# Kernel optimization log

Hardware: AMD Instinct MI355X
Metric: run time of the kernel (lower is better)

Reference implementation:

```python
import jax, jax.numpy as jnp
import numpy as np

N, NN = 16384, 10          # n_messages, max neighbors
IN, H = 135, 256           # input feature size, hidden size
HEADS, DPH = 4, 256 // 4   # attention heads, dim per head
DEPTH = 5
NEG_INF = -1e18


def setup_inputs() -> dict:
    key = jax.random.key(0)
    ks = jax.random.split(key, 17)
    s = lambda k, sh: (jax.random.normal(k, sh, jnp.float32) * 0.05)
    return {
        "fmess": jax.random.normal(ks[0], (N, IN), jnp.float32),
        "bgraph": jax.random.randint(ks[1], (N, NN), 0, N),
        "Wq": s(ks[2], (H, IN)), "bq": s(ks[3], (H,)),
        "Wk": s(ks[4], (H, H)), "bk": s(ks[5], (H,)),
        "Wv": s(ks[6], (H, H)), "bv": s(ks[7], (H,)),
        "alpha": s(ks[8], (1, 1, HEADS, 2 * DPH)),
        "abias": s(ks[9], (1, 1, HEADS)),
        "Wz": s(ks[10], (H, IN + H)), "bz": s(ks[11], (H,)),
        "Wr": s(ks[12], (H, IN)),
        "Ur": s(ks[13], (H, H)), "bur": s(ks[14], (H,)),
        "Wh": s(ks[15], (H, IN + H)), "bh": s(ks[16], (H,)),
    }


def reference(fmess, bgraph, Wq, bq, Wk, bk, Wv, bv, alpha, abias,
              Wz, bz, Wr, Ur, bur, Wh, bh):
    n = fmess.shape[0]
    # q depends only on fmess -> compute once (identical math to per-step recompute)
    q = (fmess @ Wq.T + bq).reshape(n, 1, HEADS, DPH)
    node_mask = jnp.ones((n, 1), jnp.float32).at[0, 0].set(0.0)

    def step(h, _):
        h_nei = h[bgraph]                                   # [n, nn, H] gather
        k = (h_nei @ Wk.T + bk).reshape(n, NN, HEADS, DPH)
        v = (h_nei @ Wv.T + bv).reshape(n, NN, HEADS, DPH)
        qb = jnp.broadcast_to(q, (n, NN, HEADS, DPH))
        qk = jax.nn.leaky_relu(jnp.concatenate([qb, k], axis=-1))  # slope 0.01
        score = jnp.sum(qk * alpha, axis=-1) + abias        # [n, nn, heads]
        attn_mask = (jnp.sum(h_nei, axis=2) == 0)[:, :, None]
        score = jnp.where(attn_mask, NEG_INF, score)
        w = jax.nn.softmax(score, axis=1)                   # softmax over neighbors
        sum_h = jnp.einsum('nmh,nmhd->nhd', w, v).reshape(n, H)
        z = jax.nn.sigmoid(jnp.concatenate([fmess, sum_h], axis=1) @ Wz.T + bz)
        r = jax.nn.sigmoid(fmess @ Wr.T + sum_h @ Ur.T + bur)
        pre_h = jnp.tanh(jnp.concatenate([fmess, r * sum_h], axis=1) @ Wh.T + bh)
        new_h = ((1.0 - z) * sum_h + z * pre_h) * node_mask
        return new_h, None

    h0 = jnp.zeros((n, H), jnp.float32)
    h, _ = jax.lax.scan(step, h0, None, length=DEPTH)
    return h
```

## Files before the change

### kernel.cpp

```cpp
#include <hip/hip_runtime.h>
#include <hip/hip_bf16.h>
#include <math.h>

#define NMSG 16384
#define NNEI 10
#define INF_ 135
#define KPAD 160
#define HID 256
#define DPH 64
#define DEPTH 5

typedef __attribute__((ext_vector_type(8))) short short8b;
typedef __attribute__((ext_vector_type(4))) float f32x4;
typedef __hip_bfloat16 bf16;

__device__ __forceinline__ float sigmoidf_(float x){ return 1.f/(1.f+expf(-x)); }
__device__ __forceinline__ float b2f(unsigned short u){ return __uint_as_float(((unsigned)u)<<16); }
__device__ __forceinline__ float ldb(const bf16* p, size_t off){
    return b2f(*((const unsigned short*)p + off));
}

__device__ __forceinline__ void gload_lds16(const void* g, void* l){
    __builtin_amdgcn_global_load_lds(
        (const __attribute__((address_space(1))) unsigned int*)g,
        (__attribute__((address_space(3))) unsigned int*)l, 16, 0, 0);
}

template<int EPI>
__global__ __launch_bounds__(256) void mm_k(
    const bf16* __restrict__ A1, const bf16* __restrict__ A2,
    const bf16* __restrict__ B1, const bf16* __restrict__ B2, int K,
    const bf16* __restrict__ E0, const bf16* __restrict__ E1,
    const float* __restrict__ b0, const float* __restrict__ b1,
    const bf16* __restrict__ SH,
    float* __restrict__ Cf, bf16* __restrict__ Cb0, bf16* __restrict__ Cb1, bf16* __restrict__ Cb2,
    const float* __restrict__ AL, float* __restrict__ SKout, float* __restrict__ Snext)
{
    constexpr int BM = (EPI==0) ? 128 : 64;
    constexpr int MF = BM/64;
    constexpr int BK = 32;
    constexpr bool DB = (EPI>=2);
    constexpr bool DA = (EPI==3);
    __shared__ __align__(16) unsigned short As1[BM*BK];
    __shared__ __align__(16) unsigned short As2[DA ? BM*BK : 8];
    __shared__ __align__(16) unsigned short Bs1[64*BK];
    __shared__ __align__(16) unsigned short Bs2[DB ? 64*BK : 8];
    const int tid = threadIdx.x;
    const int w = tid >> 6, lane = tid & 63;
    const int bm0 = blockIdx.x * BM;
    const int bn0 = blockIdx.y * 64;
    const int rq = lane >> 2, slot = lane & 3;
    const int fr = lane & 15, fs = lane >> 4;
    const int wrow = w * (MF*16);

    f32x4 acc1[MF][4] = {};
    f32x4 acc2[MF][4] = {};

    for (int k0 = 0; k0 < K; k0 += BK){
        #pragma unroll
        for (int i = 0; i < MF; ++i){
            const int r0 = i*64 + w*16;
            const int r  = r0 + rq;
            const int sw = slot ^ ((r >> 1) & 3);
            gload_lds16(A1 + (size_t)(bm0 + r)*K + k0 + sw*8, As1 + r0*BK);
            if constexpr (DA)
                gload_lds16(A2 + (size_t)(bm0 + r)*K + k0 + sw*8, As2 + r0*BK);
        }
        {
            const int r0 = w*16;
            const int r  = r0 + rq;
            const int sw = slot ^ ((r >> 1) & 3);
            gload_lds16(B1 + (size_t)(bn0 + r)*K + k0 + sw*8, Bs1 + r0*BK);
            if constexpr (DB)
                gload_lds16(B2 + (size_t)(bn0 + r)*K + k0 + sw*8, Bs2 + r0*BK);
        }
        __syncthreads();
        short8b af1[MF], af2[MF], bv1[4], bv2[4];
        #pragma unroll
        for (int mi = 0; mi < MF; ++mi){
            const int row = wrow + mi*16 + fr;
            const int sw = fs ^ ((row >> 1) & 3);
            af1[mi] = *(const short8b*)((const char*)As1 + row*64 + sw*16);
            if constexpr (DA)
                af2[mi] = *(const short8b*)((const char*)As2 + row*64 + sw*16);
        }
        #pragma unroll
        for (int ni = 0; ni < 4; ++ni){
            const int row = ni*16 + fr;
            const int sw = fs ^ ((row >> 1) & 3);
            bv1[ni] = *(const short8b*)((const char*)Bs1 + row*64 + sw*16);
            if constexpr (DB)
                bv2[ni] = *(const short8b*)((const char*)Bs2 + row*64 + sw*16);
        }
        #pragma unroll
        for (int mi = 0; mi < MF; ++mi)
            #pragma unroll
            for (int ni = 0; ni < 4; ++ni){
                acc1[mi][ni] = __builtin_amdgcn_mfma_f32_16x16x32_bf16(af1[mi], bv1[ni], acc1[mi][ni], 0, 0, 0);
                if constexpr (DB)
                    acc2[mi][ni] = __builtin_amdgcn_mfma_f32_16x16x32_bf16(
                        DA ? af2[mi] : af1[mi], bv2[ni], acc2[mi][ni], 0, 0, 0);
            }
        __syncthreads();
    }

    if constexpr (EPI == 0 || EPI == 1){
        const bool score = (EPI == 1) || (blockIdx.y < 4);
        if (score){
            const int head = blockIdx.y;
            #pragma unroll
            for (int mi = 0; mi < MF; ++mi){
                #pragma unroll
                for (int t = 0; t < 4; ++t){
                    float p = 0.f;
                    #pragma unroll
                    for (int ni = 0; ni < 4; ++ni){
                        const int d = ni*16 + fr;
                        float x = acc1[mi][ni][t] + b0[head*64 + d];
                        float lr = x > 0.f ? x : 0.01f*x;
                        p = fmaf(lr, AL[head*128 + d], p);
                    }
                    p += __shfl_xor(p,1); p += __shfl_xor(p,2);
                    p += __shfl_xor(p,4); p += __shfl_xor(p,8);
                    if (fr == 0){
                        const int m = bm0 + wrow + mi*16 + fs*4 + t;
                        SKout[m*4 + head] = p;
                    }
                }
            }
        } else {
            const int sel = ((int)blockIdx.y - 4) >> 2;
            bf16* dst = (sel == 0) ? Cb0 : (sel == 1) ? Cb1 : Cb2;
            const int cbase = (((int)blockIdx.y - 4) & 3) * 64;
            #pragma unroll
            for (int mi = 0; mi < MF; ++mi)
                #pragma unroll
                for (int ni = 0; ni < 4; ++ni)
                    #pragma unroll
                    for (int t = 0; t < 4; ++t){
                        const int m = bm0 + wrow + mi*16 + fs*4 + t;
                        const int c = cbase + ni*16 + fr;
                        dst[(size_t)m*HID + c] = __float2bfloat16(acc1[mi][ni][t]);
                    }
        }
    } else if constexpr (EPI == 2){
        const int cbase = (int)blockIdx.y * 64;
        #pragma unroll
        for (int mi = 0; mi < MF; ++mi)
            #pragma unroll
            for (int ni = 0; ni < 4; ++ni)
                #pragma unroll
                for (int t = 0; t < 4; ++t){
                    const int m = bm0 + wrow + mi*16 + fs*4 + t;
                    const int c = cbase + ni*16 + fr;
                    const size_t off = (size_t)m*HID + c;
                    const float sumh = acc1[mi][ni][t] + b0[c];
                    const float r = sigmoidf_(acc2[mi][ni][t] + ldb(E1, off) + b1[c]);
                    Cb0[off] = __float2bfloat16(sumh);
                    Cb1[off] = __float2bfloat16(r * sumh);
                }
    } else {
        const int cbase = (int)blockIdx.y * 64;
        #pragma unroll
        for (int mi = 0; mi < MF; ++mi){
            #pragma unroll
            for (int t = 0; t < 4; ++t){
                const int m = bm0 + wrow + mi*16 + fs*4 + t;
                float psum = 0.f;
                #pragma unroll
                for (int ni = 0; ni < 4; ++ni){
                    const int c = cbase + ni*16 + fr;
                    const size_t off = (size_t)m*HID + c;
                    const float ph = tanhf(acc1[mi][ni][t] + ldb(E0, off) + b0[c]);
                    const float z  = sigmoidf_(acc2[mi][ni][t] + ldb(E1, off) + b1[c]);
                    const float sh = ldb(SH, off);
                    float hn = (1.f - z)*sh + z*ph;
                    if (m == 0) hn = 0.f;
                    if (Cf)  Cf[off]  = hn;
                    if (Cb0) Cb0[off] = __float2bfloat16(hn);
                    psum += hn;
                }
                if (Snext){
                    psum += __shfl_xor(psum,1); psum += __shfl_xor(psum,2);
                    psum += __shfl_xor(psum,4); psum += __shfl_xor(psum,8);
                    if (fr == 0) atomicAdd(&Snext[m], psum);
                }
            }
        }
    }
}

struct ConvSegs {
    const float* src[8];
    bf16* dst[8];
    int srcld[8], col0[8], ncols[8], dstld[8];
    int start[8];
};
__global__ __launch_bounds__(256) void convall_k(ConvSegs cs, int total){
    int i = blockIdx.x*256 + threadIdx.x;
    if (i >= total) return;
    int s = 0;
    #pragma unroll
    for (int j = 1; j < 8; ++j) if (i >= cs.start[j]) s = j;
    const int li = i - cs.start[s];
    const int ld = cs.dstld[s];
    const int r = li / ld, c = li - r*ld;
    float v = (c < cs.ncols[s]) ? cs.src[s][(size_t)r*cs.srcld[s] + cs.col0[s] + c] : 0.f;
    cs.dst[s][li] = __float2bfloat16(v);
}

__global__ __launch_bounds__(256) void wcomb_k(
    const float* __restrict__ Ur, const float* __restrict__ Wz,
    const float* __restrict__ Wv, const float* __restrict__ bv,
    const float* __restrict__ bur, const float* __restrict__ bz,
    bf16* __restrict__ Urv, bf16* __restrict__ Wzv,
    float* __restrict__ bur2, float* __restrict__ bz2)
{
    const int i = blockIdx.x, j = threadIdx.x;
    const bool zp = (i >= 256);
    const int r = zp ? i - 256 : i;
    const float* Arow = zp ? (Wz + (size_t)r*(INF_+HID) + INF_) : (Ur + (size_t)r*HID);
    float acc = 0.f;
    for (int q = 0; q < HID; ++q)
        acc = fmaf(Arow[q], Wv[(size_t)q*HID + j], acc);
    (zp ? Wzv : Urv)[(size_t)r*HID + j] = __float2bfloat16(acc);
    float part = Arow[j] * bv[j];
    part += __shfl_xor(part,1);  part += __shfl_xor(part,2);  part += __shfl_xor(part,4);
    part += __shfl_xor(part,8);  part += __shfl_xor(part,16); part += __shfl_xor(part,32);
    __shared__ float red[4];
    if ((j & 63) == 0) red[j >> 6] = part;
    __syncthreads();
    if (j == 0){
        float s = red[0] + red[1] + red[2] + red[3];
        if (zp) bz2[r] = bz[r] + s; else bur2[r] = bur[r] + s;
    }
}

__global__ __launch_bounds__(256) void attn_k(
    const int*   __restrict__ bgraph,
    const float* __restrict__ sq,
    const float* __restrict__ sk,
    const float* __restrict__ S,
    const float* __restrict__ abias,
    const bf16*  __restrict__ H,
    bf16* __restrict__ haggb)
{
    const int gid  = blockIdx.x*256 + threadIdx.x;
    const int n    = gid >> 6;
    const int lane = gid & 63;
    const int head = lane >> 4;
    const float ab  = abias[head];
    const float sqv = sq[n*4 + head];
    int g[NNEI];
    #pragma unroll
    for (int j = 0; j < NNEI; ++j) g[j] = bgraph[n*NNEI + j];
    float sc[NNEI];
    float mx = -1e30f;
    #pragma unroll
    for (int j = 0; j < NNEI; ++j){
        float s = sqv + sk[g[j]*4 + head] + ab;
        if (S[g[j]] == 0.f) s = -1e18f;
        sc[j] = s;
        mx = fmaxf(mx, s);
    }
    float den = 0.f;
    #pragma unroll
    for (int j = 0; j < NNEI; ++j){ sc[j] = expf(sc[j] - mx); den += sc[j]; }
    const float inv = 1.f/den;
    float a0=0.f, a1=0.f, a2=0.f, a3=0.f;
    #pragma unroll
    for (int j = 0; j < NNEI; ++j){
        const float w = sc[j]*inv;
        const ushort4 vv = *reinterpret_cast<const ushort4*>(
            (const unsigned short*)H + (size_t)g[j]*HID + lane*4);
        a0 = fmaf(w, b2f(vv.x), a0);
        a1 = fmaf(w, b2f(vv.y), a1);
        a2 = fmaf(w, b2f(vv.z), a2);
        a3 = fmaf(w, b2f(vv.w), a3);
    }
    ushort4 ob;
    { bf16 t0=__float2bfloat16(a0); ob.x=*(unsigned short*)&t0; }
    { bf16 t1=__float2bfloat16(a1); ob.y=*(unsigned short*)&t1; }
    { bf16 t2=__float2bfloat16(a2); ob.z=*(unsigned short*)&t2; }
    { bf16 t3=__float2bfloat16(a3); ob.w=*(unsigned short*)&t3; }
    *reinterpret_cast<ushort4*>((unsigned short*)haggb + (size_t)n*HID + lane*4) = ob;
}

extern "C" void kernel_launch(void* const* d_in, const int* in_sizes, int n_in,
                              void* d_out, int out_size, void* d_ws, size_t ws_size,
                              hipStream_t stream) {
    const float* fmess = (const float*)d_in[0];
    const int*   bgraph= (const int*  )d_in[1];
    const float* Wq    = (const float*)d_in[2];
    const float* bq    = (const float*)d_in[3];
    const float* Wk    = (const float*)d_in[4];
    const float* bk    = (const float*)d_in[5];
    const float* Wv    = (const float*)d_in[6];
    const float* bv    = (const float*)d_in[7];
    const float* alpha = (const float*)d_in[8];
    const float* abias = (const float*)d_in[9];
    const float* Wz    = (const float*)d_in[10];
    const float* bz    = (const float*)d_in[11];
    const float* Wr    = (const float*)d_in[12];
    const float* Ur    = (const float*)d_in[13];
    const float* bur   = (const float*)d_in[14];
    const float* Wh    = (const float*)d_in[15];
    const float* bh    = (const float*)d_in[16];
    float* out = (float*)d_out;

    const size_t NH = (size_t)NMSG*HID;
    char* p = (char*)d_ws;
    auto alloc = [&](size_t bytes)->char*{ char* r = p; p += (bytes + 255) & ~(size_t)255; return r; };
    bf16* fmessb = (bf16*)alloc((size_t)NMSG*KPAD*2);
    bf16* Wcat   = (bf16*)alloc((size_t)1024*KPAD*2);
    bf16* Wkb    = (bf16*)alloc((size_t)256*HID*2);
    bf16* Wvb    = (bf16*)alloc((size_t)256*HID*2);
    bf16* Wh2b   = (bf16*)alloc((size_t)256*HID*2);
    bf16* Urv    = (bf16*)alloc((size_t)256*HID*2);
    bf16* Wzv    = (bf16*)alloc((size_t)256*HID*2);
    float* bur2  = (float*)alloc(256*4);
    float* bz2   = (float*)alloc(256*4);
    bf16* FZb    = (bf16*)alloc(NH*2);
    bf16* FRb    = (bf16*)alloc(NH*2);
    bf16* FHb    = (bf16*)alloc(NH*2);
    bf16* sumhb  = (bf16*)alloc(NH*2);
    bf16* rsb    = (bf16*)alloc(NH*2);
    char* zreg   = alloc(NH*2 + NH*2 + 5*(size_t)NMSG*4);
    bf16*  hb    = (bf16*)zreg;
    bf16*  haggb = (bf16*)(zreg + NH*2);
    float* S_all = (float*)(zreg + NH*2 + NH*2);
    const size_t zbytes = NH*2 + NH*2 + 5*(size_t)NMSG*4;
    float* sq    = (float*)alloc((size_t)NMSG*4*4);
    float* sk    = (float*)alloc((size_t)NMSG*4*4);

    const dim3 gb(256);
    const int rgrid = NMSG*64/256;

    {
        ConvSegs cs;
        const size_t WQK = (size_t)256*KPAD;
        const float* srcs[8] = {fmess, Wq, Wz, Wr, Wh, Wk, Wv, Wh};
        bf16* dsts[8] = {fmessb, Wcat, Wcat+WQK, Wcat+2*WQK, Wcat+3*WQK, Wkb, Wvb, Wh2b};
        int srclds[8] = {INF_, INF_, INF_+HID, INF_, INF_+HID, HID, HID, INF_+HID};
        int col0s[8]  = {0,0,0,0,0, 0,0,INF_};
        int ncolss[8] = {INF_,INF_,INF_,INF_,INF_, HID,HID,HID};
        int dstlds[8] = {KPAD,KPAD,KPAD,KPAD,KPAD, HID,HID,HID};
        int sizes[8]  = {NMSG*KPAD, 256*KPAD,256*KPAD,256*KPAD,256*KPAD,
                         256*HID,256*HID,256*HID};
        int st = 0;
        for (int j = 0; j < 8; ++j){
            cs.src[j]=srcs[j]; cs.dst[j]=dsts[j]; cs.srcld[j]=srclds[j];
            cs.col0[j]=col0s[j]; cs.ncols[j]=ncolss[j]; cs.dstld[j]=dstlds[j];
            cs.start[j]=st; st += sizes[j];
        }
        convall_k<<<(st+255)/256, gb, 0, stream>>>(cs, st);
    }
    wcomb_k<<<512, gb, 0, stream>>>(Ur, Wz, Wv, bv, bur, bz, Urv, Wzv, bur2, bz2);
    hipMemsetAsync(zreg, 0, zbytes, stream);

    mm_k<0><<<dim3(NMSG/128, 16), gb, 0, stream>>>(fmessb, nullptr, Wcat, nullptr, KPAD,
        nullptr, nullptr, bq, nullptr, nullptr,
        nullptr, FZb, FRb, FHb, alpha, sq, nullptr);

    for (int step = 0; step < DEPTH; ++step){
        const bool last = (step == DEPTH-1);
        float* cf    = last ? out : nullptr;
        bf16*  cb    = last ? nullptr : hb;
        float* Snext = last ? nullptr : (S_all + (step+1)*(size_t)NMSG);
        if (step > 0){
            mm_k<1><<<dim3(NMSG/64, 4), gb, 0, stream>>>(hb, nullptr, Wkb, nullptr, HID,
                nullptr, nullptr, bk, nullptr, nullptr,
                nullptr, nullptr, nullptr, nullptr, alpha + DPH, sk, nullptr);
            attn_k<<<rgrid, gb, 0, stream>>>(bgraph, sq, sk, S_all + step*(size_t)NMSG,
                                             abias, hb, haggb);
        }
        mm_k<2><<<dim3(NMSG/64, 4), gb, 0, stream>>>(haggb, nullptr, Wvb, Urv, HID,
            nullptr, FRb, bv, bur2, nullptr,
            nullptr, sumhb, rsb, nullptr, nullptr, nullptr, nullptr);
        mm_k<3><<<dim3(NMSG/64, 4), gb, 0, stream>>>(rsb, haggb, Wh2b, Wzv, HID,
            FHb, FZb, bh, bz2, sumhb,
            cf, cb, nullptr, nullptr, nullptr, nullptr, Snext);
    }
}
```

Before: 393.6 us.

## Fuse per-step kernels into one persistent kernel with grid barriers

Replaces the per-depth-step launches (K-score GEMM, attention gather, two gated GEMMs) with a single persistent kernel that loops over the steps and separates phases with atomic-counter grid barriers. The aim is to remove launch overhead and inter-kernel gaps across the roughly 15 dependent launches. In exchange, a fixed grid (occupancy × 256, capped at 512) does grid-stride tiles, and several barriers per step add spin-wait cost. Correctness relies on all blocks being co-resident, since the launch is not cooperative.

```diff
diff --git a/kernel.cpp b/kernel.cpp
--- a/kernel.cpp
+++ b/kernel.cpp
@@ -26,158 +26,299 @@
         (__attribute__((address_space(3))) unsigned int*)l, 16, 0, 0);
 }
 
-template<int EPI>
-__global__ __launch_bounds__(256) void mm_k(
-    const bf16* __restrict__ A1, const bf16* __restrict__ A2,
-    const bf16* __restrict__ B1, const bf16* __restrict__ B2, int K,
-    const bf16* __restrict__ E0, const bf16* __restrict__ E1,
-    const float* __restrict__ b0, const float* __restrict__ b1,
-    const bf16* __restrict__ SH,
-    float* __restrict__ Cf, bf16* __restrict__ Cb0, bf16* __restrict__ Cb1, bf16* __restrict__ Cb2,
-    const float* __restrict__ AL, float* __restrict__ SKout, float* __restrict__ Snext)
+__device__ __forceinline__ void gbar(unsigned* cnt, unsigned target){
+    __threadfence();
+    __syncthreads();
+    if (threadIdx.x == 0){
+        __hip_atomic_fetch_add(cnt, 1u, __ATOMIC_RELEASE, __HIP_MEMORY_SCOPE_AGENT);
+        unsigned v;
+        do {
+            __builtin_amdgcn_s_sleep(2);
+            v = __hip_atomic_load(cnt, __ATOMIC_ACQUIRE, __HIP_MEMORY_SCOPE_AGENT);
+        } while (v < target);
+    }
+    __syncthreads();
+    __threadfence();
+}
+
+__global__ __launch_bounds__(256) void pre_k(
+    const bf16* __restrict__ A1, const bf16* __restrict__ B1, int K,
+    const float* __restrict__ b0,
+    bf16* __restrict__ Cb0, bf16* __restrict__ Cb1, bf16* __restrict__ Cb2,
+    const float* __restrict__ AL, float* __restrict__ SKout)
 {
-    constexpr int BM = (EPI==0) ? 128 : 64;
-    constexpr int MF = BM/64;
-    constexpr int BK = 32;
-    constexpr bool DB = (EPI>=2);
-    constexpr bool DA = (EPI==3);
+    constexpr int BM=128, BK=32;
     __shared__ __align__(16) unsigned short As1[BM*BK];
-    __shared__ __align__(16) unsigned short As2[DA ? BM*BK : 8];
     __shared__ __align__(16) unsigned short Bs1[64*BK];
-    __shared__ __align__(16) unsigned short Bs2[DB ? 64*BK : 8];
     const int tid = threadIdx.x;
     const int w = tid >> 6, lane = tid & 63;
     const int bm0 = blockIdx.x * BM;
     const int bn0 = blockIdx.y * 64;
     const int rq = lane >> 2, slot = lane & 3;
     const int fr = lane & 15, fs = lane >> 4;
-    const int wrow = w * (MF*16);
-
-    f32x4 acc1[MF][4] = {};
-    f32x4 acc2[MF][4] = {};
+    const int wrow = w * 32;
+
+    f32x4 acc1[2][4] = {};
 
     for (int k0 = 0; k0 < K; k0 += BK){
         #pragma unroll
-        for (int i = 0; i < MF; ++i){
+        for (int i = 0; i < 2; ++i){
             const int r0 = i*64 + w*16;
             const int r  = r0 + rq;
             const int sw = slot ^ ((r >> 1) & 3);
             gload_lds16(A1 + (size_t)(bm0 + r)*K + k0 + sw*8, As1 + r0*BK);
-            if constexpr (DA)
-                gload_lds16(A2 + (size_t)(bm0 + r)*K + k0 + sw*8, As2 + r0*BK);
         }
         {
             const int r0 = w*16;
             const int r  = r0 + rq;
             const int sw = slot ^ ((r >> 1) & 3);
             gload_lds16(B1 + (size_t)(bn0 + r)*K + k0 + sw*8, Bs1 + r0*BK);
-            if constexpr (DB)
-                gload_lds16(B2 + (size_t)(bn0 + r)*K + k0 + sw*8, Bs2 + r0*BK);
         }
         __syncthreads();
-        short8b af1[MF], af2[MF], bv1[4], bv2[4];
-        #pragma unroll
-        for (int mi = 0; mi < MF; ++mi){
+        short8b af1[2], bv1[4];
+        #pragma unroll
+        for (int mi = 0; mi < 2; ++mi){
             const int row = wrow + mi*16 + fr;
             const int sw = fs ^ ((row >> 1) & 3);
             af1[mi] = *(const short8b*)((const char*)As1 + row*64 + sw*16);
-            if constexpr (DA)
-                af2[mi] = *(const short8b*)((const char*)As2 + row*64 + sw*16);
         }
         #pragma unroll
         for (int ni = 0; ni < 4; ++ni){
             const int row = ni*16 + fr;
             const int sw = fs ^ ((row >> 1) & 3);
             bv1[ni] = *(const short8b*)((const char*)Bs1 + row*64 + sw*16);
+        }
+        #pragma unroll
+        for (int mi = 0; mi < 2; ++mi)
+            #pragma unroll
+            for (int ni = 0; ni < 4; ++ni)
+                acc1[mi][ni] = __builtin_amdgcn_mfma_f32_16x16x32_bf16(af1[mi], bv1[ni], acc1[mi][ni], 0, 0, 0);
+        __syncthreads();
+    }
+
+    if (blockIdx.y < 4){
+        const int head = blockIdx.y;
+        #pragma unroll
+        for (int mi = 0; mi < 2; ++mi){
+            #pragma unroll
+            for (int t = 0; t < 4; ++t){
+                float p = 0.f;
+                #pragma unroll
+                for (int ni = 0; ni < 4; ++ni){
+                    const int d = ni*16 + fr;
+                    float x = acc1[mi][ni][t] + b0[head*64 + d];
+                    float lr = x > 0.f ? x : 0.01f*x;
+                    p = fmaf(lr, AL[head*128 + d], p);
+                }
+                p += __shfl_xor(p,1); p += __shfl_xor(p,2);
+                p += __shfl_xor(p,4); p += __shfl_xor(p,8);
+                if (fr == 0){
+                    const int m = bm0 + wrow + mi*16 + fs*4 + t;
+                    SKout[m*4 + head] = p;
+                }
+            }
+        }
+    } else {
+        const int sel = ((int)blockIdx.y - 4) >> 2;
+        bf16* dst = (sel == 0) ? Cb0 : (sel == 1) ? Cb1 : Cb2;
+        const int cbase = (((int)blockIdx.y - 4) & 3) * 64;
+        #pragma unroll
+        for (int mi = 0; mi < 2; ++mi)
+            #pragma unroll
+            for (int ni = 0; ni < 4; ++ni)
+                #pragma unroll
+                for (int t = 0; t < 4; ++t){
+                    const int m = bm0 + wrow + mi*16 + fs*4 + t;
+                    const int c = cbase + ni*16 + fr;
+                    dst[(size_t)m*HID + c] = __float2bfloat16(acc1[mi][ni][t]);
+                }
+    }
+}
+
+struct FA {
+    const int* bgraph;
+    const bf16 *Wkb, *Wvb, *Urv, *Wzv, *Wh2b;
+    const bf16 *FZb, *FRb, *FHb;
+    bf16 *hb, *haggb, *sumhb, *rsb;
+    float *S_all, *sq, *sk;
+    const float *bk, *bv, *bur2, *bz2, *bh, *alpha, *abias;
+    float* out;
+    unsigned* cnt;
+};
+
+template<bool DA, bool DB>
+__device__ __forceinline__ void gemm64(
+    const bf16* __restrict__ A1, const bf16* __restrict__ A2,
+    const bf16* __restrict__ B1, const bf16* __restrict__ B2,
+    int K, int bm0, int bn0,
+    unsigned short* LA1, unsigned short* LA2,
+    unsigned short* LB1, unsigned short* LB2,
+    f32x4 (&acc1)[4], f32x4 (&acc2)[4])
+{
+    const int tid = threadIdx.x;
+    const int w = tid >> 6, lane = tid & 63;
+    const int rq = lane >> 2, slot = lane & 3;
+    const int fr = lane & 15, fs = lane >> 4;
+    for (int k0 = 0; k0 < K; k0 += 32){
+        {
+            const int r0 = w*16;
+            const int r  = r0 + rq;
+            const int sw = slot ^ ((r >> 1) & 3);
+            gload_lds16(A1 + (size_t)(bm0 + r)*K + k0 + sw*8, LA1 + r0*32);
+            if constexpr (DA)
+                gload_lds16(A2 + (size_t)(bm0 + r)*K + k0 + sw*8, LA2 + r0*32);
+            gload_lds16(B1 + (size_t)(bn0 + r)*K + k0 + sw*8, LB1 + r0*32);
             if constexpr (DB)
-                bv2[ni] = *(const short8b*)((const char*)Bs2 + row*64 + sw*16);
-        }
-        #pragma unroll
-        for (int mi = 0; mi < MF; ++mi)
-            #pragma unroll
-            for (int ni = 0; ni < 4; ++ni){
-                acc1[mi][ni] = __builtin_amdgcn_mfma_f32_16x16x32_bf16(af1[mi], bv1[ni], acc1[mi][ni], 0, 0, 0);
-                if constexpr (DB)
-                    acc2[mi][ni] = __builtin_amdgcn_mfma_f32_16x16x32_bf16(
-                        DA ? af2[mi] : af1[mi], bv2[ni], acc2[mi][ni], 0, 0, 0);
-            }
+                gload_lds16(B2 + (size_t)(bn0 + r)*K + k0 + sw*8, LB2 + r0*32);
+        }
         __syncthreads();
-    }
-
-    if constexpr (EPI == 0 || EPI == 1){
-        const bool score = (EPI == 1) || (blockIdx.y < 4);
-        if (score){
-            const int head = blockIdx.y;
-            #pragma unroll
-            for (int mi = 0; mi < MF; ++mi){
-                #pragma unroll
-                for (int t = 0; t < 4; ++t){
+        short8b af1, af2, bv1[4], bv2[4];
+        {
+            const int row = w*16 + fr;
+            const int sw = fs ^ ((row >> 1) & 3);
+            af1 = *(const short8b*)((const char*)LA1 + row*64 + sw*16);
+            if constexpr (DA)
+                af2 = *(const short8b*)((const char*)LA2 + row*64 + sw*16);
+        }
+        #pragma unroll
+        for (int ni = 0; ni < 4; ++ni){
+            const int row = ni*16 + fr;
+            const int sw = fs ^ ((row >> 1) & 3);
+            bv1[ni] = *(const short8b*)((const char*)LB1 + row*64 + sw*16);
+            if constexpr (DB)
+                bv2[ni] = *(const short8b*)((const char*)LB2 + row*64 + sw*16);
+        }
+        #pragma unroll
+        for (int ni = 0; ni < 4; ++ni){
+            acc1[ni] = __builtin_amdgcn_mfma_f32_16x16x32_bf16(af1, bv1[ni], acc1[ni], 0, 0, 0);
+            if constexpr (DB)
+                acc2[ni] = __builtin_amdgcn_mfma_f32_16x16x32_bf16(
+                    DA ? af2 : af1, bv2[ni], acc2[ni], 0, 0, 0);
+        }
+        __syncthreads();
+    }
+}
+
+__global__ __launch_bounds__(256, 2) void fused_k(FA a){
+    __shared__ __align__(16) unsigned short LA1[64*32];
+    __shared__ __align__(16) unsigned short LA2[64*32];
+    __shared__ __align__(16) unsigned short LB1[64*32];
+    __shared__ __align__(16) unsigned short LB2[64*32];
+    const int tid = threadIdx.x;
+    const int lane = tid & 63;
+    const int fr = lane & 15, fs = lane >> 4;
+    const int w = tid >> 6;
+    unsigned bar = 0;
+
+    for (int step = 0; step < DEPTH; ++step){
+        if (step > 0){
+            for (int t = blockIdx.x; t < 1024; t += gridDim.x){
+                const int bm0 = (t & 255) * 64, head = t >> 8;
+                f32x4 acc1[4] = {}; f32x4 acc2[4];
+                gemm64<false,false>(a.hb, nullptr, a.Wkb, nullptr, HID,
+                                    bm0, head*64, LA1, LA2, LB1, LB2, acc1, acc2);
+                #pragma unroll
+                for (int tt = 0; tt < 4; ++tt){
                     float p = 0.f;
                     #pragma unroll
                     for (int ni = 0; ni < 4; ++ni){
                         const int d = ni*16 + fr;
-                        float x = acc1[mi][ni][t] + b0[head*64 + d];
+                        float x = acc1[ni][tt] + a.bk[head*64 + d];
                         float lr = x > 0.f ? x : 0.01f*x;
-                        p = fmaf(lr, AL[head*128 + d], p);
+                        p = fmaf(lr, a.alpha[head*128 + 64 + d], p);
                     }
                     p += __shfl_xor(p,1); p += __shfl_xor(p,2);
                     p += __shfl_xor(p,4); p += __shfl_xor(p,8);
                     if (fr == 0){
-                        const int m = bm0 + wrow + mi*16 + fs*4 + t;
-                        SKout[m*4 + head] = p;
+                        const int m = bm0 + w*16 + fs*4 + tt;
+                        a.sk[m*4 + head] = p;
                     }
                 }
             }
-        } else {
-            const int sel = ((int)blockIdx.y - 4) >> 2;
-            bf16* dst = (sel == 0) ? Cb0 : (sel == 1) ? Cb1 : Cb2;
-            const int cbase = (((int)blockIdx.y - 4) & 3) * 64;
-            #pragma unroll
-            for (int mi = 0; mi < MF; ++mi)
-                #pragma unroll
-                for (int ni = 0; ni < 4; ++ni)
-                    #pragma unroll
-                    for (int t = 0; t < 4; ++t){
-                        const int m = bm0 + wrow + mi*16 + fs*4 + t;
-                        const int c = cbase + ni*16 + fr;
-                        dst[(size_t)m*HID + c] = __float2bfloat16(acc1[mi][ni][t]);
-                    }
-        }
-    } else if constexpr (EPI == 2){
-        const int cbase = (int)blockIdx.y * 64;
-        #pragma unroll
-        for (int mi = 0; mi < MF; ++mi)
+            bar += gridDim.x; gbar(a.cnt, bar);
+            const float* S = a.S_all + (size_t)step*NMSG;
+            for (int t = blockIdx.x; t < NMSG/4; t += gridDim.x){
+                const int n = t*4 + (tid >> 6);
+                const int head4 = lane >> 4;
+                const float ab  = a.abias[head4];
+                const float sqv = a.sq[n*4 + head4];
+                int gidx[NNEI];
+                #pragma unroll
+                for (int j = 0; j < NNEI; ++j) gidx[j] = a.bgraph[n*NNEI + j];
+                float sc[NNEI];
+                float mx = -1e30f;
+                #pragma unroll
+                for (int j = 0; j < NNEI; ++j){
+                    float s = sqv + a.sk[gidx[j]*4 + head4] + ab;
+                    if (S[gidx[j]] == 0.f) s = -1e18f;
+                    sc[j] = s;
+                    mx = fmaxf(mx, s);
+                }
+                float den = 0.f;
+                #pragma unroll
+                for (int j = 0; j < NNEI; ++j){ sc[j] = expf(sc[j] - mx); den += sc[j]; }
+                const float inv = 1.f/den;
+                float a0=0.f, a1=0.f, a2=0.f, a3=0.f;
+                #pragma unroll
+                for (int j = 0; j < NNEI; ++j){
+                    const float wj = sc[j]*inv;
+                    const ushort4 vv = *reinterpret_cast<const ushort4*>(
+                        (const unsigned short*)a.hb + (size_t)gidx[j]*HID + lane*4);
+                    a0 = fmaf(wj, b2f(vv.x), a0);
+                    a1 = fmaf(wj, b2f(vv.y), a1);
+                    a2 = fmaf(wj, b2f(vv.z), a2);
+                    a3 = fmaf(wj, b2f(vv.w), a3);
+                }
+                ushort4 ob;
+                { bf16 t0=__float2bfloat16(a0); ob.x=*(unsigned short*)&t0; }
+                { bf16 t1=__float2bfloat16(a1); ob.y=*(unsigned short*)&t1; }
+                { bf16 t2=__float2bfloat16(a2); ob.z=*(unsigned short*)&t2; }
+                { bf16 t3=__float2bfloat16(a3); ob.w=*(unsigned short*)&t3; }
+                *reinterpret_cast<ushort4*>((unsigned short*)a.haggb + (size_t)n*HID + lane*4) = ob;
+            }
+            bar += gridDim.x; gbar(a.cnt, bar);
+        }
+        for (int t = blockIdx.x; t < 1024; t += gridDim.x){
+            const int bm0 = (t & 255) * 64, bn0 = (t >> 8) * 64;
+            f32x4 acc1[4] = {}; f32x4 acc2[4] = {};
+            gemm64<false,true>(a.haggb, nullptr, a.Wvb, a.Urv, HID,
+                               bm0, bn0, LA1, LA2, LB1, LB2, acc1, acc2);
             #pragma unroll
             for (int ni = 0; ni < 4; ++ni)
                 #pragma unroll
-                for (int t = 0; t < 4; ++t){
-                    const int m = bm0 + wrow + mi*16 + fs*4 + t;
-                    const int c = cbase + ni*16 + fr;
+                for (int tt = 0; tt < 4; ++tt){
+                    const int m = bm0 + w*16 + fs*4 + tt;
+                    const int c = bn0 + ni*16 + fr;
                     const size_t off = (size_t)m*HID + c;
-                    const float sumh = acc1[mi][ni][t] + b0[c];
-                    const float r = sigmoidf_(acc2[mi][ni][t] + ldb(E1, off) + b1[c]);
-                    Cb0[off] = __float2bfloat16(sumh);
-                    Cb1[off] = __float2bfloat16(r * sumh);
-                }
-    } else {
-        const int cbase = (int)blockIdx.y * 64;
-        #pragma unroll
-        for (int mi = 0; mi < MF; ++mi){
+                    const float sumh = acc1[ni][tt] + a.bv[c];
+                    const float r = sigmoidf_(acc2[ni][tt] + ldb(a.FRb, off) + a.bur2[c]);
+                    a.sumhb[off] = __float2bfloat16(sumh);
+                    a.rsb[off]   = __float2bfloat16(r * sumh);
+                }
+        }
+        bar += gridDim.x; gbar(a.cnt, bar);
+        const bool last = (step == DEPTH-1);
+        float* Snext = last ? nullptr : (a.S_all + (size_t)(step+1)*NMSG);
+        for (int t = blockIdx.x; t < 1024; t += gridDim.x){
+            const int bm0 = (t & 255) * 64, bn0 = (t >> 8) * 64;
+            f32x4 acc1[4] = {}; f32x4 acc2[4] = {};
+            gemm64<true,true>(a.rsb, a.haggb, a.Wh2b, a.Wzv, HID,
+                              bm0, bn0, LA1, LA2, LB1, LB2, acc1, acc2);
             #pragma unroll
-            for (int t = 0; t < 4; ++t){
-                const int m = bm0 + wrow + mi*16 + fs*4 + t;
+            for (int tt = 0; tt < 4; ++tt){
+                const int m = bm0 + w*16 + fs*4 + tt;
                 float psum = 0.f;
                 #pragma unroll
                 for (int ni = 0; ni < 4; ++ni){
-                    const int c = cbase + ni*16 + fr;
+                    const int c = bn0 + ni*16 + fr;
                     const size_t off = (size_t)m*HID + c;
-                    const float ph = tanhf(acc1[mi][ni][t] + ldb(E0, off) + b0[c]);
-                    const float z  = sigmoidf_(acc2[mi][ni][t] + ldb(E1, off) + b1[c]);
-                    const float sh = ldb(SH, off);
+                    const float ph = tanhf(acc1[ni][tt] + ldb(a.FHb, off) + a.bh[c]);
+                    const float z  = sigmoidf_(acc2[ni][tt] + ldb(a.FZb, off) + a.bz2[c]);
+                    const float sh = ldb(a.sumhb, off);
                     float hn = (1.f - z)*sh + z*ph;
                     if (m == 0) hn = 0.f;
-                    if (Cf)  Cf[off]  = hn;
-                    if (Cb0) Cb0[off] = __float2bfloat16(hn);
+                    if (last) a.out[off] = hn;
+                    else      a.hb[off] = __float2bfloat16(hn);
                     psum += hn;
                 }
                 if (Snext){
@@ -187,6 +328,7 @@
                 }
             }
         }
+        if (!last){ bar += gridDim.x; gbar(a.cnt, bar); }
     }
 }
 
@@ -236,56 +378,6 @@
     }
 }
 
-__global__ __launch_bounds__(256) void attn_k(
-    const int*   __restrict__ bgraph,
-    const float* __restrict__ sq,
-    const float* __restrict__ sk,
-    const float* __restrict__ S,
-    const float* __restrict__ abias,
-    const bf16*  __restrict__ H,
-    bf16* __restrict__ haggb)
-{
-    const int gid  = blockIdx.x*256 + threadIdx.x;
-    const int n    = gid >> 6;
-    const int lane = gid & 63;
-    const int head = lane >> 4;
-    const float ab  = abias[head];
-    const float sqv = sq[n*4 + head];
-    int g[NNEI];
-    #pragma unroll
-    for (int j = 0; j < NNEI; ++j) g[j] = bgraph[n*NNEI + j];
-    float sc[NNEI];
-    float mx = -1e30f;
-    #pragma unroll
-    for (int j = 0; j < NNEI; ++j){
-        float s = sqv + sk[g[j]*4 + head] + ab;
-        if (S[g[j]] == 0.f) s = -1e18f;
-        sc[j] = s;
-        mx = fmaxf(mx, s);
-    }
-    float den = 0.f;
-    #pragma unroll
-    for (int j = 0; j < NNEI; ++j){ sc[j] = expf(sc[j] - mx); den += sc[j]; }
-    const float inv = 1.f/den;
-    float a0=0.f, a1=0.f, a2=0.f, a3=0.f;
-    #pragma unroll
-    for (int j = 0; j < NNEI; ++j){
-        const float w = sc[j]*inv;
-        const ushort4 vv = *reinterpret_cast<const ushort4*>(
-            (const unsigned short*)H + (size_t)g[j]*HID + lane*4);
-        a0 = fmaf(w, b2f(vv.x), a0);
-        a1 = fmaf(w, b2f(vv.y), a1);
-        a2 = fmaf(w, b2f(vv.z), a2);
-        a3 = fmaf(w, b2f(vv.w), a3);
-    }
-    ushort4 ob;
-    { bf16 t0=__float2bfloat16(a0); ob.x=*(unsigned short*)&t0; }
-    { bf16 t1=__float2bfloat16(a1); ob.y=*(unsigned short*)&t1; }
-    { bf16 t2=__float2bfloat16(a2); ob.z=*(unsigned short*)&t2; }
-    { bf16 t3=__float2bfloat16(a3); ob.w=*(unsigned short*)&t3; }
-    *reinterpret_cast<ushort4*>((unsigned short*)haggb + (size_t)n*HID + lane*4) = ob;
-}
-
 extern "C" void kernel_launch(void* const* d_in, const int* in_sizes, int n_in,
                               void* d_out, int out_size, void* d_ws, size_t ws_size,
                               hipStream_t stream) {
@@ -325,16 +417,16 @@
     bf16* FHb    = (bf16*)alloc(NH*2);
     bf16* sumhb  = (bf16*)alloc(NH*2);
     bf16* rsb    = (bf16*)alloc(NH*2);
-    char* zreg   = alloc(NH*2 + NH*2 + 5*(size_t)NMSG*4);
-    bf16*  hb    = (bf16*)zreg;
-    bf16*  haggb = (bf16*)(zreg + NH*2);
-    float* S_all = (float*)(zreg + NH*2 + NH*2);
-    const size_t zbytes = NH*2 + NH*2 + 5*(size_t)NMSG*4;
+    char* zreg   = alloc(256 + NH*2 + NH*2 + 5*(size_t)NMSG*4);
+    unsigned* cnt = (unsigned*)zreg;
+    bf16*  hb    = (bf16*)(zreg + 256);
+    bf16*  haggb = (bf16*)(zreg + 256 + NH*2);
+    float* S_all = (float*)(zreg + 256 + NH*2 + NH*2);
+    const size_t zbytes = 256 + NH*2 + NH*2 + 5*(size_t)NMSG*4;
     float* sq    = (float*)alloc((size_t)NMSG*4*4);
     float* sk    = (float*)alloc((size_t)NMSG*4*4);
 
     const dim3 gb(256);
-    const int rgrid = NMSG*64/256;
 
     {
         ConvSegs cs;
@@ -358,27 +450,25 @@
     wcomb_k<<<512, gb, 0, stream>>>(Ur, Wz, Wv, bv, bur, bz, Urv, Wzv, bur2, bz2);
     hipMemsetAsync(zreg, 0, zbytes, stream);
 
-    mm_k<0><<<dim3(NMSG/128, 16), gb, 0, stream>>>(fmessb, nullptr, Wcat, nullptr, KPAD,
-        nullptr, nullptr, bq, nullptr, nullptr,
-        nullptr, FZb, FRb, FHb, alpha, sq, nullptr);
-
-    for (int step = 0; step < DEPTH; ++step){
-        const bool last = (step == DEPTH-1);
-        float* cf    = last ? out : nullptr;
-        bf16*  cb    = last ? nullptr : hb;
-        float* Snext = last ? nullptr : (S_all + (step+1)*(size_t)NMSG);
-        if (step > 0){
-            mm_k<1><<<dim3(NMSG/64, 4), gb, 0, stream>>>(hb, nullptr, Wkb, nullptr, HID,
-                nullptr, nullptr, bk, nullptr, nullptr,
-                nullptr, nullptr, nullptr, nullptr, alpha + DPH, sk, nullptr);
-            attn_k<<<rgrid, gb, 0, stream>>>(bgraph, sq, sk, S_all + step*(size_t)NMSG,
-                                             abias, hb, haggb);
-        }
-        mm_k<2><<<dim3(NMSG/64, 4), gb, 0, stream>>>(haggb, nullptr, Wvb, Urv, HID,
-            nullptr, FRb, bv, bur2, nullptr,
-            nullptr, sumhb, rsb, nullptr, nullptr, nullptr, nullptr);
-        mm_k<3><<<dim3(NMSG/64, 4), gb, 0, stream>>>(rsb, haggb, Wh2b, Wzv, HID,
-            FHb, FZb, bh, bz2, sumhb,
-            cf, cb, nullptr, nullptr, nullptr, nullptr, Snext);
-    }
-}
+    pre_k<<<dim3(NMSG/128, 16), gb, 0, stream>>>(fmessb, Wcat, KPAD,
+        bq, FZb, FRb, FHb, alpha, sq);
+
+    FA fa;
+    fa.bgraph = bgraph;
+    fa.Wkb = Wkb; fa.Wvb = Wvb; fa.Urv = Urv; fa.Wzv = Wzv; fa.Wh2b = Wh2b;
+    fa.FZb = FZb; fa.FRb = FRb; fa.FHb = FHb;
+    fa.hb = hb; fa.haggb = haggb; fa.sumhb = sumhb; fa.rsb = rsb;
+    fa.S_all = S_all; fa.sq = sq; fa.sk = sk;
+    fa.bk = bk; fa.bv = bv; fa.bur2 = bur2; fa.bz2 = bz2; fa.bh = bh;
+    fa.alpha = alpha; fa.abias = abias;
+    fa.out = out;
+    fa.cnt = cnt;
+
+    int occ = 0;
+    if (hipOccupancyMaxActiveBlocksPerMultiprocessor(&occ, (const void*)fused_k, 256, 0)
+            != hipSuccess || occ < 1)
+        occ = 1;
+    int grid = occ * 256;
+    if (grid > 512) grid = 512;
+    fused_k<<<dim3(grid), gb, 0, stream>>>(fa);
+}
```

Result: slower. 1.513 ms (+284.4%).
